# Kernel tuning notes

Measured on AMD Instinct MI355X. Metric: run time of the kernel, lower is better.

## Reference

```python
import jax, jax.numpy as jnp
import numpy as np

H = 8                 # num_heads
SCALE = 25.0          # self.scale
SIM_THRESH = 0.75
CONF_SIM_THRESH = 0.99


def _l2n(x):
    return x / jnp.linalg.norm(x, axis=-1, keepdims=True)


def setup_inputs() -> dict:
    key = jax.random.key(0)
    ks = jax.random.split(key, 10)
    B, N1, N2, C = 1, 512, 2048, 1024
    s = 0.02
    return {
        'x_cls': jax.random.normal(ks[0], (B, N2, C), jnp.float32),
        'x_reg': jax.random.normal(ks[1], (B, N2, C), jnp.float32),
        'cls_score': jax.random.uniform(ks[2], (N2,), dtype=jnp.float32),
        'fg_score': jax.random.uniform(ks[3], (N2,), dtype=jnp.float32),
        'W_q_cls': jax.random.normal(ks[4], (C, C), jnp.float32) * s,
        'W_kv_cls': jax.random.normal(ks[5], (C, 2 * C), jnp.float32) * s,
        'W_q_reg': jax.random.normal(ks[6], (C, C), jnp.float32) * s,
        'W_kv_reg': jax.random.normal(ks[7], (C, 2 * C), jnp.float32) * s,
        'W_lin': jax.random.normal(ks[8], (2 * C, 2 * C), jnp.float32) * s,
        'b_lin': jnp.zeros((2 * C,), jnp.float32),
        'W_lin_reg': jax.random.normal(ks[9], (2 * C, 2 * C), jnp.float32) * s,
        'b_lin_reg': jnp.zeros((2 * C,), jnp.float32),
        'local_preds_num': 512,
    }


def _forward(x_cls, x_reg, cls_score, fg_score, W_q_cls, W_kv_cls, W_q_reg, W_kv_reg,
             W_lin, b_lin, W_lin_reg, b_lin_reg, N1):
    B, N2, C = x_cls.shape
    hd = C // H
    # QKV projections (torch Linear with bias=False; weights stored [in,out])
    q_cls = (x_cls[:, :N1] @ W_q_cls).reshape(B, N1, H, hd).transpose(0, 2, 1, 3)   # [B,H,N1,hd]
    kv = (x_cls @ W_kv_cls).reshape(B, N2, 2, H, hd).transpose(2, 0, 3, 1, 4)
    k_cls, v_cls = kv[0], kv[1]                                                      # [B,H,N2,hd]
    q_reg = (x_reg[:, :N1] @ W_q_reg).reshape(B, N1, H, hd).transpose(0, 2, 1, 3)
    kv = (x_reg @ W_kv_reg).reshape(B, N2, 2, H, hd).transpose(2, 0, 3, 1, 4)
    k_reg, v_reg = kv[0], kv[1]
    # L2 normalization of q, k and of v for raw similarity
    q_cls, k_cls = _l2n(q_cls), _l2n(k_cls)
    q_reg, k_reg = _l2n(q_reg), _l2n(k_reg)
    v_cls_n, v_reg_n = _l2n(v_cls), _l2n(v_reg)
    # per-key score broadcast over [1,H,N1,N2] (use_mask=False path)
    cs = cls_score.reshape(1, 1, 1, N2)
    # raw value-value similarity
    attn_cls_raw = jnp.einsum('bhqd,bhkd->bhqk', v_cls_n[:, :, :N1], v_cls_n)        # [B,H,N1,N2]
    attn_reg_raw = jnp.einsum('bhqd,bhkd->bhqk', v_reg_n[:, :, :N1], v_reg_n)
    # blended softmax attention (attn_drop=0 -> identity)
    attn_cls = jax.nn.softmax(jnp.einsum('bhqd,bhkd->bhqk', q_cls, k_cls) * SCALE * cs, axis=-1)
    attn_reg = jax.nn.softmax(jnp.einsum('bhqd,bhkd->bhqk', q_reg, k_reg) * SCALE, axis=-1)
    attn = (attn_cls + attn_reg) * 0.5
    # attended features + original local values, then output linears
    x = jnp.einsum('bhqk,bhkd->bhqd', attn, v_cls).transpose(0, 2, 1, 3).reshape(B, N1, C)
    x_ori = v_cls[:, :, :N1].transpose(0, 2, 1, 3).reshape(B, N1, C)
    out_cls = jnp.concatenate([x, x_ori], axis=-1) @ W_lin + b_lin                   # [B,N1,2C]
    xr = jnp.einsum('bhqk,bhkd->bhqd', attn, v_reg).transpose(0, 2, 1, 3).reshape(B, N1, C)
    xr_ori = v_reg[:, :, :N1].transpose(0, 2, 1, 3).reshape(B, N1, C)
    out_reg = jnp.concatenate([xr, xr_ori], axis=-1) @ W_lin_reg + b_lin_reg         # reconf=True
    # ave branch: similarity-masked renormalized second-round averaging (batch 0)
    sim_mask = (attn_cls_raw.sum(axis=1)[0] / H > SIM_THRESH).astype(x_cls.dtype)    # [N1,N2]
    obj_mask = (attn_reg_raw.sum(axis=1)[0] / H > CONF_SIM_THRESH).astype(x_cls.dtype)
    sim_round2 = jax.nn.softmax(attn.sum(axis=1)[0] / H, axis=-1)
    sim_round2 = sim_mask * sim_round2
    sim_round2 = sim_round2 / sim_round2.sum(axis=-1, keepdims=True)
    obj_w = obj_mask * sim_round2
    obj_w = obj_w / obj_w.sum(axis=-1, keepdims=True)
    support_cls = v_cls.transpose(0, 2, 1, 3).reshape(B, N2, C)[0]                   # [N2,C]
    support_reg = v_reg.transpose(0, 2, 1, 3).reshape(B, N2, C)[0]
    cls_feature = jnp.concatenate([sim_round2 @ support_cls, out_cls[0]], axis=-1)   # [N1,3C]
    reg_feature = jnp.concatenate([obj_w @ support_reg, out_reg[0]], axis=-1)        # [N1,3C]
    return cls_feature, reg_feature


def reference(x_cls, x_reg, cls_score, fg_score, W_q_cls, W_kv_cls, W_q_reg, W_kv_reg,
              W_lin, b_lin, W_lin_reg, b_lin_reg, local_preds_num):
    return _forward(x_cls, x_reg, cls_score, fg_score, W_q_cls, W_kv_cls, W_q_reg,
                    W_kv_reg, W_lin, b_lin, W_lin_reg, b_lin_reg, local_preds_num)
```

## Files before the change

### kernel.cpp

```cpp
#include <hip/hip_runtime.h>

typedef _Float16 half8 __attribute__((ext_vector_type(8)));
typedef _Float16 half4v __attribute__((ext_vector_type(4)));
typedef float f32x4 __attribute__((ext_vector_type(4)));

#define GLD16(gptr, lptr) \
    __builtin_amdgcn_global_load_lds((const __attribute__((address_space(1))) void*)(gptr), \
                                     (__attribute__((address_space(3))) void*)(lptr), 16, 0, 0)

#define WAIT_VM3   0x0F73
#define WAIT_VM0   0x0F70
#define WAIT_LGKM0 0xC07F

struct GD {
    const _Float16* A; const _Float16* B; void* C;
    const float* colScale;
    _Float16 *vnp, *vtp, *xop;
    long sAh, sAg, sBh, sBg, sSplit, sCh, sCg;
    int lda, ldb, ldc, K, SK, hmask, hshift;
    int ahx, outHalf, csMode, nx, ny, normMode;
    float alpha;
};

__global__ __launch_bounds__(512, 4)
void hgemm3(GD d0, GD d1, int zSplit)
{
    const bool second = (int)blockIdx.z >= zSplit;
    const GD& d = second ? d1 : d0;
    const int bz = second ? (int)blockIdx.z - zSplit : (int)blockIdx.z;
    const int bx = (int)blockIdx.x, by = (int)blockIdx.y;
    if (bx >= d.nx || by >= d.ny) return;

    __shared__ uint4 smem[4608];
    char* sb = (char*)smem;
    const int tid = threadIdx.x;
    const int w = tid >> 6, l = tid & 63;
    const int m0 = by << 8, n0 = bx << 7;
    const int wm = (w >> 1) << 6, wn = (w & 1) << 6;
    const int kq = l >> 4, lm = l & 15;

    const int zz = bz / d.SK, s = bz - zz * d.SK;
    const int h = d.ahx ? bx : (zz & d.hmask);
    const int g = d.ahx ? zz : (zz >> d.hshift);
    const _Float16* A = d.A + (long)h * d.sAh + (long)g * d.sAg;
    const _Float16* B = d.B + (long)h * d.sBh + (long)g * d.sBg;
    const long Coff = (long)s * d.sSplit + (long)h * d.sCh + (long)g * d.sCg;
    const int kper = d.K / d.SK, kbeg = s * kper;
    const int NT = kper >> 5;

    const int rS = (w << 4) + (l >> 2);
    const int cS = (l & 3) ^ ((l >> 3) & 3);
    const _Float16* gA0 = A + (long)(m0 + rS) * d.lda + kbeg + cS * 8;
    const _Float16* gB0 = B + (long)(n0 + rS) * d.ldb + kbeg + cS * 8;
    const int lo = w * 1024 + l * 16;

    auto stage = [&](int t) {
        char* dst = sb + (t % 3) * 24576;
        GLD16(gA0 + t * 32,                     dst + lo);
        GLD16(gA0 + (long)128 * d.lda + t * 32, dst + 8192 + lo);
        GLD16(gB0 + t * 32,                     dst + 16384 + lo);
    };

    f32x4 acc[4][4] = {};
    stage(0);
    if (NT > 1) stage(1);
    if (NT > 1) __builtin_amdgcn_s_waitcnt(WAIT_VM3);
    else        __builtin_amdgcn_s_waitcnt(WAIT_VM0);
    __builtin_amdgcn_s_barrier();

    const int sw16 = ((kq ^ ((lm >> 1) & 3)) << 4);
    for (int t = 0; t < NT; ++t) {
        const char* cb = sb + (t % 3) * 24576;
        const char* pa = cb + (wm + lm) * 64 + sw16;
        const char* pb = cb + 16384 + (wn + lm) * 64 + sw16;
        half8 af[4], bfr[4];
        bfr[0] = *(const half8*)(pb + 0 * 1024);
        bfr[1] = *(const half8*)(pb + 1 * 1024);
        #pragma unroll
        for (int i = 0; i < 4; ++i) af[i] = *(const half8*)(pa + i * 1024);
        if (t + 2 < NT) stage(t + 2);
        __builtin_amdgcn_s_waitcnt(WAIT_LGKM0);
        __builtin_amdgcn_sched_barrier(0);
        __builtin_amdgcn_s_setprio(1);
        #pragma unroll
        for (int mi = 0; mi < 4; ++mi) {
            acc[mi][0] = __builtin_amdgcn_mfma_f32_16x16x32_f16(af[mi], bfr[0], acc[mi][0], 0, 0, 0);
            acc[mi][1] = __builtin_amdgcn_mfma_f32_16x16x32_f16(af[mi], bfr[1], acc[mi][1], 0, 0, 0);
        }
        __builtin_amdgcn_s_setprio(0);
        bfr[2] = *(const half8*)(pb + 2 * 1024);
        bfr[3] = *(const half8*)(pb + 3 * 1024);
        if (t + 2 < NT)      __builtin_amdgcn_s_waitcnt(WAIT_VM3);
        else if (t + 1 < NT) __builtin_amdgcn_s_waitcnt(WAIT_VM0);
        __builtin_amdgcn_s_waitcnt(WAIT_LGKM0);
        __builtin_amdgcn_sched_barrier(0);
        __builtin_amdgcn_s_setprio(1);
        #pragma unroll
        for (int mi = 0; mi < 4; ++mi) {
            acc[mi][2] = __builtin_amdgcn_mfma_f32_16x16x32_f16(af[mi], bfr[2], acc[mi][2], 0, 0, 0);
            acc[mi][3] = __builtin_amdgcn_mfma_f32_16x16x32_f16(af[mi], bfr[3], acc[mi][3], 0, 0, 0);
        }
        __builtin_amdgcn_s_setprio(0);
        __builtin_amdgcn_s_barrier();
    }

    if (d.normMode == 0) {
        const int rbase = m0 + wm + kq * 4;
        #pragma unroll
        for (int mi = 0; mi < 4; ++mi) {
            #pragma unroll
            for (int ni = 0; ni < 4; ++ni) {
                const int col = n0 + wn + ni * 16 + lm;
                float cs = d.alpha;
                if (d.csMode == 1 || (d.csMode == 2 && g == 0)) cs *= d.colScale[col];
                #pragma unroll
                for (int r = 0; r < 4; ++r) {
                    const long row = rbase + mi * 16 + r;
                    const float v = acc[mi][ni][r] * cs;
                    const long off = Coff + row * d.ldc + col;
                    if (d.outHalf) ((_Float16*)d.C)[off] = (_Float16)v;
                    else           ((float*)d.C)[off] = v;
                }
            }
        }
        return;
    }

    float* part = (float*)sb;
    float ssq[4][4];
    #pragma unroll
    for (int mi = 0; mi < 4; ++mi)
        #pragma unroll
        for (int r = 0; r < 4; ++r) {
            float sq = 0.f;
            #pragma unroll
            for (int ni = 0; ni < 4; ++ni) { const float v = acc[mi][ni][r]; sq += v * v; }
            sq += __shfl_xor(sq, 1, 64);
            sq += __shfl_xor(sq, 2, 64);
            sq += __shfl_xor(sq, 4, 64);
            sq += __shfl_xor(sq, 8, 64);
            ssq[mi][r] = sq;
        }
    if (lm == 0) {
        #pragma unroll
        for (int mi = 0; mi < 4; ++mi)
            #pragma unroll
            for (int r = 0; r < 4; ++r)
                part[(w & 1) * 256 + wm + kq * 4 + mi * 16 + r] = ssq[mi][r];
    }
    __syncthreads();

    #pragma unroll
    for (int mi = 0; mi < 4; ++mi) {
        #pragma unroll
        for (int r = 0; r < 4; ++r) {
            const int rl = wm + kq * 4 + mi * 16 + r;
            const float inv = rsqrtf(part[rl] + part[256 + rl]);
            const long rg = m0 + rl;
            if (d.normMode == 1) {
                #pragma unroll
                for (int ni = 0; ni < 4; ++ni) {
                    const int col = n0 + wn + ni * 16 + lm;
                    ((_Float16*)d.C)[(long)g * 524288 + rg * 1024 + col] =
                        (_Float16)(acc[mi][ni][r] * inv);
                }
            } else if (n0 < 1024) {
                #pragma unroll
                for (int ni = 0; ni < 4; ++ni) {
                    const int col = n0 + wn + ni * 16 + lm;
                    ((_Float16*)d.C)[(long)g * 2097152 + rg * 1024 + col] =
                        (_Float16)(acc[mi][ni][r] * inv);
                }
            } else {
                #pragma unroll
                for (int ni = 0; ni < 4; ++ni) {
                    const int nL = n0 - 1024 + wn + ni * 16 + lm;
                    d.vnp[(long)g * 2097152 + rg * 1024 + nL] =
                        (_Float16)(acc[mi][ni][r] * inv);
                    if (rg < 512)
                        d.xop[(long)g * 524288 + rg * 1024 + nL] = (_Float16)acc[mi][ni][r];
                }
            }
        }
    }
    if (d.normMode == 2 && n0 >= 1024) {
        #pragma unroll
        for (int mi = 0; mi < 4; ++mi)
            #pragma unroll
            for (int ni = 0; ni < 4; ++ni) {
                const int nL = n0 - 1024 + wn + ni * 16 + lm;
                half4v t;
                t.x = (_Float16)acc[mi][ni][0]; t.y = (_Float16)acc[mi][ni][1];
                t.z = (_Float16)acc[mi][ni][2]; t.w = (_Float16)acc[mi][ni][3];
                *(half4v*)(d.vtp + (long)g * 2097152 + (long)nL * 2048
                           + m0 + wm + kq * 4 + mi * 16) = t;
            }
    }
}

static GD mkgd(const _Float16* A, const _Float16* B, void* C, const float* cscale,
               long sAh, long sAg, long sBh, long sBg, long sSplit, long sCh, long sCg,
               int lda, int ldb, int ldc, int K, int SK, int hmask, int hshift,
               int ahx, int outHalf, int csMode, int nx, int ny, float alpha)
{
    GD d; d.A=A; d.B=B; d.C=C; d.colScale=cscale;
    d.vnp=nullptr; d.vtp=nullptr; d.xop=nullptr;
    d.sAh=sAh; d.sAg=sAg; d.sBh=sBh; d.sBg=sBg; d.sSplit=sSplit; d.sCh=sCh; d.sCg=sCg;
    d.lda=lda; d.ldb=ldb; d.ldc=ldc; d.K=K; d.SK=SK; d.hmask=hmask; d.hshift=hshift;
    d.ahx=ahx; d.outHalf=outHalf; d.csMode=csMode; d.nx=nx; d.ny=ny; d.normMode=0;
    d.alpha=alpha;
    return d;
}

__global__ __launch_bounds__(256)
void prep_all(const float* __restrict__ x_cls, const float* __restrict__ x_reg,
              const float* __restrict__ Wq_c, const float* __restrict__ Wq_r,
              const float* __restrict__ Wkv_c, const float* __restrict__ Wkv_r,
              const float* __restrict__ Wl_c, const float* __restrict__ Wl_r,
              _Float16* __restrict__ xbf,
              _Float16* __restrict__ WqT, _Float16* __restrict__ WkvT,
              _Float16* __restrict__ WlinT)
{
    const int z = blockIdx.z;
    if (z == 6) {
        const int lin = blockIdx.y * 64 + blockIdx.x;
        const int which = lin >> 11;
        const int i = (lin & 2047) * 256 + threadIdx.x;
        const float* s = which ? x_reg : x_cls;
        const float4 v = ((const float4*)s)[i];
        half4v o;
        o.x = (_Float16)v.x; o.y = (_Float16)v.y; o.z = (_Float16)v.z; o.w = (_Float16)v.w;
        ((half4v*)(xbf + (size_t)which * 2097152))[i] = o;
        return;
    }
    __shared__ float t[32][33];
    const float* src; _Float16* dst; int ldsrc, lddst, nx, ky;
    switch (z) {
        case 0: src=Wq_c;  dst=WqT;            ldsrc=1024; lddst=1024; nx=32; ky=32; break;
        case 1: src=Wq_r;  dst=WqT+1048576;    ldsrc=1024; lddst=1024; nx=32; ky=32; break;
        case 2: src=Wkv_c; dst=WkvT;           ldsrc=2048; lddst=1024; nx=64; ky=32; break;
        case 3: src=Wkv_r; dst=WkvT+2097152;   ldsrc=2048; lddst=1024; nx=64; ky=32; break;
        case 4: src=Wl_c;  dst=WlinT;          ldsrc=2048; lddst=2048; nx=64; ky=64; break;
        default:src=Wl_r;  dst=WlinT+4194304;  ldsrc=2048; lddst=2048; nx=64; ky=64; break;
    }
    if ((int)blockIdx.x >= nx || (int)blockIdx.y >= ky) return;
    const int n0 = blockIdx.x << 5, k0 = blockIdx.y << 5;
    const int tx = threadIdx.x & 31, ty = threadIdx.x >> 5;
    #pragma unroll
    for (int j = ty; j < 32; j += 8)
        t[j][tx] = src[(size_t)(k0 + j) * ldsrc + n0 + tx];
    __syncthreads();
    #pragma unroll
    for (int j = ty; j < 32; j += 8)
        dst[(size_t)(n0 + j) * lddst + k0 + tx] = (_Float16)t[tx][j];
}

template<int OP>
__device__ __forceinline__ float bred(float v, float* lds)
{
    #pragma unroll
    for (int o = 32; o > 0; o >>= 1) {
        const float u = __shfl_xor(v, o, 64);
        v = OP ? fmaxf(v, u) : v + u;
    }
    __syncthreads();
    if ((threadIdx.x & 63) == 0) lds[threadIdx.x >> 6] = v;
    __syncthreads();
    return OP ? fmaxf(fmaxf(lds[0], lds[1]), fmaxf(lds[2], lds[3]))
              : lds[0] + lds[1] + lds[2] + lds[3];
}

template<int OP>
__device__ __forceinline__ void bred2(float& a, float& b, float* lds)
{
    #pragma unroll
    for (int o = 32; o > 0; o >>= 1) {
        const float ua = __shfl_xor(a, o, 64);
        const float ub = __shfl_xor(b, o, 64);
        a = OP ? fmaxf(a, ua) : a + ua;
        b = OP ? fmaxf(b, ub) : b + ub;
    }
    __syncthreads();
    if ((threadIdx.x & 63) == 0) {
        const int wi = threadIdx.x >> 6;
        lds[wi] = a; lds[4 + wi] = b;
    }
    __syncthreads();
    a = OP ? fmaxf(fmaxf(lds[0], lds[1]), fmaxf(lds[2], lds[3]))
           : lds[0] + lds[1] + lds[2] + lds[3];
    b = OP ? fmaxf(fmaxf(lds[4], lds[5]), fmaxf(lds[6], lds[7]))
           : lds[4] + lds[5] + lds[6] + lds[7];
}

__global__ __launch_bounds__(256)
void sb2_kernel(const _Float16* __restrict__ S16, const float* __restrict__ simPart,
                _Float16* __restrict__ attn,
                _Float16* __restrict__ wc, _Float16* __restrict__ wr)
{
    __shared__ float lds[8];
    const int q = blockIdx.x, t = threadIdx.x;
    const int c0 = t * 8;
    float asum[8] = {};
    for (int hh = 0; hh < 8; ++hh) {
        const size_t rb = (size_t)(hh * 512 + q) * 2048 + c0;
        const half8 hc = *(const half8*)(S16 + rb);
        const half8 hr = *(const half8*)(S16 + 8388608 + rb);
        float vc[8], vr[8];
        float mc = -1e30f, mr = -1e30f;
        #pragma unroll
        for (int j = 0; j < 8; ++j) {
            vc[j] = (float)hc[j]; vr[j] = (float)hr[j];
            mc = fmaxf(mc, vc[j]); mr = fmaxf(mr, vr[j]);
        }
        bred2<1>(mc, mr, lds);
        float sc = 0.f, sr = 0.f;
        #pragma unroll
        for (int j = 0; j < 8; ++j) {
            vc[j] = expf(vc[j] - mc); sc += vc[j];
            vr[j] = expf(vr[j] - mr); sr += vr[j];
        }
        bred2<0>(sc, sr, lds);
        const float ic = 0.5f / sc, ir = 0.5f / sr;
        half8 oa;
        #pragma unroll
        for (int j = 0; j < 8; ++j) {
            const float a = vc[j] * ic + vr[j] * ir;
            oa[j] = (_Float16)a;
            asum[j] += a;
        }
        *(half8*)(attn + rb) = oa;
    }
    float mx = -1e30f;
    #pragma unroll
    for (int j = 0; j < 8; ++j) { asum[j] *= 0.125f; mx = fmaxf(mx, asum[j]); }
    mx = bred<1>(mx, lds);
    const size_t qb = (size_t)q * 2048 + c0;
    const float4 sa = *(const float4*)(simPart + qb);
    const float4 sb_ = *(const float4*)(simPart + qb + 4);
    const float4 ra = *(const float4*)(simPart + 1048576 + qb);
    const float4 rb_ = *(const float4*)(simPart + 1048576 + qb + 4);
    const float sim[8] = {sa.x, sa.y, sa.z, sa.w, sb_.x, sb_.y, sb_.z, sb_.w};
    const float reg[8] = {ra.x, ra.y, ra.z, ra.w, rb_.x, rb_.y, rb_.z, rb_.w};
    float em[8], emo[8];
    float s1 = 0.f, s2 = 0.f;
    #pragma unroll
    for (int j = 0; j < 8; ++j) {
        const float e = expf(asum[j] - mx);
        const float m  = sim[j] > 0.75f ? 1.f : 0.f;
        const float mo = reg[j] > 0.99f ? 1.f : 0.f;
        em[j] = e * m; emo[j] = e * m * mo;
        s1 += em[j]; s2 += emo[j];
    }
    bred2<0>(s1, s2, lds);
    const float i1 = 1.f / s1, i2 = 1.f / s2;
    half8 o1, o2;
    #pragma unroll
    for (int j = 0; j < 8; ++j) {
        o1[j] = (_Float16)(em[j] * i1);
        o2[j] = (_Float16)(emo[j] * i2);
    }
    *(half8*)(wc + qb) = o1;
    *(half8*)(wr + qb) = o2;
}

__global__ __launch_bounds__(256)
void build_xcat(const _Float16* __restrict__ xcatPart, const _Float16* __restrict__ x_ori,
                _Float16* __restrict__ xcat)
{
    const int v8 = blockIdx.x * 256 + threadIdx.x;
    const size_t base = (size_t)v8 * 8;
    const int j = (int)(base & 2047);
    const int n = (int)((base >> 11) & 511);
    const int g = (int)(base >> 20);
    half8 o;
    if (j < 1024) {
        const size_t p = (size_t)g * 524288 + (size_t)n * 1024 + j;
        float a[8] = {};
        #pragma unroll
        for (int s = 0; s < 4; ++s) {
            const half8 v = *(const half8*)(xcatPart + (size_t)s * 1048576 + p);
            #pragma unroll
            for (int k = 0; k < 8; ++k) a[k] += (float)v[k];
        }
        #pragma unroll
        for (int k = 0; k < 8; ++k) o[k] = (_Float16)a[k];
    } else {
        o = *(const half8*)(x_ori + (size_t)g * 524288 + (size_t)n * 1024 + (j - 1024));
    }
    *(half8*)(xcat + base) = o;
}

__global__ __launch_bounds__(256)
void finalize(const float* __restrict__ avePart, const float* __restrict__ outPart,
              const float* __restrict__ b_lin, const float* __restrict__ b_lin_reg,
              float* __restrict__ out)
{
    const int v4 = blockIdx.x * 256 + threadIdx.x;
    const size_t base = (size_t)v4 * 4;
    const int c = (int)(base % 3072);
    const int r = (int)((base / 3072) & 511);
    const int g = (int)(base / (3072 * 512));
    float4 v;
    if (c < 1024) {
        const size_t p = (size_t)g * 524288 + (size_t)r * 1024 + c;
        v = make_float4(0.f, 0.f, 0.f, 0.f);
        #pragma unroll
        for (int s = 0; s < 4; ++s) {
            const float4 u = *(const float4*)(avePart + (size_t)s * 1048576 + p);
            v.x += u.x; v.y += u.y; v.z += u.z; v.w += u.w;
        }
    } else {
        const int cc = c - 1024;
        v = *(const float4*)((g ? b_lin_reg : b_lin) + cc);
        const size_t p = (size_t)g * 1048576 + (size_t)r * 2048 + cc;
        #pragma unroll
        for (int s = 0; s < 4; ++s) {
            const float4 u = *(const float4*)(outPart + (size_t)s * 2097152 + p);
            v.x += u.x; v.y += u.y; v.z += u.z; v.w += u.w;
        }
    }
    *(float4*)(out + base) = v;
}

extern "C" void kernel_launch(void* const* d_in, const int* in_sizes, int n_in,
                              void* d_out, int out_size, void* d_ws, size_t ws_size,
                              hipStream_t stream)
{
    const float* x_cls     = (const float*)d_in[0];
    const float* x_reg     = (const float*)d_in[1];
    const float* cls_score = (const float*)d_in[2];
    const float* W_q_cls   = (const float*)d_in[4];
    const float* W_kv_cls  = (const float*)d_in[5];
    const float* W_q_reg   = (const float*)d_in[6];
    const float* W_kv_reg  = (const float*)d_in[7];
    const float* W_lin     = (const float*)d_in[8];
    const float* b_lin     = (const float*)d_in[9];
    const float* W_lin_reg = (const float*)d_in[10];
    const float* b_lin_reg = (const float*)d_in[11];
    float* out = (float*)d_out;

    if (ws_size < (size_t)124 * 1048576) return;

    char* W = (char*)d_ws;
    auto at = [&](size_t mb) { return (void*)(W + mb * 1048576); };
    _Float16* WlinT   = (_Float16*)at(0);
    _Float16* vT      = (_Float16*)at(16);
    _Float16* x_ori   = (_Float16*)at(24);
    _Float16* w_c     = (_Float16*)at(26);
    _Float16* w_r     = (_Float16*)at(28);
    _Float16* qn      = (_Float16*)at(30);
    float*    simPart = (float*)at(32);
    float*    outPart = (float*)at(32);
    _Float16* kn      = (_Float16*)at(40);
    _Float16* vn      = (_Float16*)at(48);
    _Float16* attn_h  = (_Float16*)at(40);
    _Float16* xbf     = (_Float16*)at(56);
    _Float16* WqT     = (_Float16*)at(64);
    _Float16* xcat16  = (_Float16*)at(64);
    _Float16* WkvT    = (_Float16*)at(68);
    _Float16* S16     = (_Float16*)at(76);
    _Float16* xcatPart= (_Float16*)at(76);
    float*    avePart = (float*)at(84);

    prep_all<<<dim3(64, 64, 7), 256, 0, stream>>>(
        x_cls, x_reg, W_q_cls, W_q_reg, W_kv_cls, W_kv_reg, W_lin, W_lin_reg,
        xbf, WqT, WkvT, WlinT);

    {
        GD q  = mkgd(xbf, WqT, qn, nullptr,
                     0, 2097152, 0, 1048576, 0, 0, 0,
                     1024, 1024, 1024, 1024, 1, 0, 0, 1, 0, 0, 8, 2, 1.f);
        q.normMode = 1;
        GD kv = mkgd(xbf, WkvT, kn, nullptr,
                     0, 2097152, 0, 2097152, 0, 0, 0,
                     1024, 1024, 1024, 1024, 1, 0, 0, 1, 0, 0, 16, 8, 1.f);
        kv.normMode = 2; kv.vnp = vn; kv.vtp = vT; kv.xop = x_ori;
        hgemm3<<<dim3(16, 8, 4), 512, 0, stream>>>(q, kv, 2);
    }

    {
        GD vs = mkgd(vn, vn, simPart, nullptr,
                     0, 2097152, 0, 2097152, 0, 0, 1048576,
                     1024, 1024, 2048, 1024, 1, 0, 0, 0, 0, 0, 16, 2, 0.125f);
        GD sc = mkgd(qn, kn, S16, cls_score,
                     128, 524288, 128, 2097152, 0, 1048576, 8388608,
                     1024, 1024, 2048, 128, 1, 7, 3, 0, 1, 2, 16, 2, 25.f);
        hgemm3<<<dim3(16, 2, 18), 512, 0, stream>>>(vs, sc, 2);
    }

    sb2_kernel<<<512, 256, 0, stream>>>(S16, simPart, attn_h, w_c, w_r);

    {
        GD av = mkgd(attn_h, vT, xcatPart, nullptr,
                     1048576, 0, 0, 2097152, 1048576, 0, 524288,
                     2048, 2048, 1024, 2048, 4, 0, 0, 1, 1, 0, 8, 2, 1.f);
        GD ae = mkgd(w_c, vT, avePart, nullptr,
                     0, 1048576, 0, 2097152, 1048576, 0, 524288,
                     2048, 2048, 1024, 2048, 4, 0, 0, 0, 0, 0, 8, 2, 1.f);
        hgemm3<<<dim3(8, 2, 16), 512, 0, stream>>>(av, ae, 8);
    }

    build_xcat<<<1024, 256, 0, stream>>>(xcatPart, x_ori, xcat16);

    {
        GD ol = mkgd(xcat16, WlinT, outPart, nullptr,
                     0, 1048576, 0, 4194304, 2097152, 0, 1048576,
                     2048, 2048, 2048, 2048, 4, 0, 0, 0, 0, 0, 16, 2, 1.f);
        hgemm3<<<dim3(16, 2, 8), 512, 0, stream>>>(ol, ol, 8);
    }

    finalize<<<3072, 256, 0, stream>>>(avePart, outPart, b_lin, b_lin_reg, out);
}
```

Baseline: 270.1 us.

## Write x_ori directly into xcat buffer and simplify GEMM main loop schedule

The KV projection epilogue now writes the unnormalized V rows straight into the right half of the concatenated xcat buffer, so build_xcat only reduces the split-K partials into the left half. This drops the separate x_ori buffer and halves build_xcat's grid and traffic. The GEMM inner loop is also rewritten to load all A/B fragments at once and issue all 16 MFMAs together. It drops the split half-step schedule, sched_barriers and setprio, and issues the next stage's global loads after the MFMAs instead of before them. That may reduce overlap between LDS reads, global prefetch and MFMA work.

```diff
diff --git a/kernel.cpp b/kernel.cpp
--- a/kernel.cpp
+++ b/kernel.cpp
@@ -71,36 +71,22 @@
     const int sw16 = ((kq ^ ((lm >> 1) & 3)) << 4);
     for (int t = 0; t < NT; ++t) {
         const char* cb = sb + (t % 3) * 24576;
+        half8 af[4], bfr[4];
         const char* pa = cb + (wm + lm) * 64 + sw16;
         const char* pb = cb + 16384 + (wn + lm) * 64 + sw16;
-        half8 af[4], bfr[4];
-        bfr[0] = *(const half8*)(pb + 0 * 1024);
-        bfr[1] = *(const half8*)(pb + 1 * 1024);
-        #pragma unroll
-        for (int i = 0; i < 4; ++i) af[i] = *(const half8*)(pa + i * 1024);
-        if (t + 2 < NT) stage(t + 2);
+        #pragma unroll
+        for (int i = 0; i < 4; ++i) {
+            af[i]  = *(const half8*)(pa + i * 1024);
+            bfr[i] = *(const half8*)(pb + i * 1024);
+        }
+        #pragma unroll
+        for (int mi = 0; mi < 4; ++mi)
+            #pragma unroll
+            for (int ni = 0; ni < 4; ++ni)
+                acc[mi][ni] = __builtin_amdgcn_mfma_f32_16x16x32_f16(af[mi], bfr[ni], acc[mi][ni], 0, 0, 0);
         __builtin_amdgcn_s_waitcnt(WAIT_LGKM0);
-        __builtin_amdgcn_sched_barrier(0);
-        __builtin_amdgcn_s_setprio(1);
-        #pragma unroll
-        for (int mi = 0; mi < 4; ++mi) {
-            acc[mi][0] = __builtin_amdgcn_mfma_f32_16x16x32_f16(af[mi], bfr[0], acc[mi][0], 0, 0, 0);
-            acc[mi][1] = __builtin_amdgcn_mfma_f32_16x16x32_f16(af[mi], bfr[1], acc[mi][1], 0, 0, 0);
-        }
-        __builtin_amdgcn_s_setprio(0);
-        bfr[2] = *(const half8*)(pb + 2 * 1024);
-        bfr[3] = *(const half8*)(pb + 3 * 1024);
-        if (t + 2 < NT)      __builtin_amdgcn_s_waitcnt(WAIT_VM3);
+        if (t + 2 < NT) { stage(t + 2); __builtin_amdgcn_s_waitcnt(WAIT_VM3); }
         else if (t + 1 < NT) __builtin_amdgcn_s_waitcnt(WAIT_VM0);
-        __builtin_amdgcn_s_waitcnt(WAIT_LGKM0);
-        __builtin_amdgcn_sched_barrier(0);
-        __builtin_amdgcn_s_setprio(1);
-        #pragma unroll
-        for (int mi = 0; mi < 4; ++mi) {
-            acc[mi][2] = __builtin_amdgcn_mfma_f32_16x16x32_f16(af[mi], bfr[2], acc[mi][2], 0, 0, 0);
-            acc[mi][3] = __builtin_amdgcn_mfma_f32_16x16x32_f16(af[mi], bfr[3], acc[mi][3], 0, 0, 0);
-        }
-        __builtin_amdgcn_s_setprio(0);
         __builtin_amdgcn_s_barrier();
     }
 
@@ -178,7 +164,8 @@
                     d.vnp[(long)g * 2097152 + rg * 1024 + nL] =
                         (_Float16)(acc[mi][ni][r] * inv);
                     if (rg < 512)
-                        d.xop[(long)g * 524288 + rg * 1024 + nL] = (_Float16)acc[mi][ni][r];
+                        d.xop[((long)g * 512 + rg) * 2048 + 1024 + nL] =
+                            (_Float16)acc[mi][ni][r];
                 }
             }
         }
@@ -364,30 +351,24 @@
 }
 
 __global__ __launch_bounds__(256)
-void build_xcat(const _Float16* __restrict__ xcatPart, const _Float16* __restrict__ x_ori,
-                _Float16* __restrict__ xcat)
+void build_xcat(const _Float16* __restrict__ xcatPart, _Float16* __restrict__ xcat)
 {
     const int v8 = blockIdx.x * 256 + threadIdx.x;
-    const size_t base = (size_t)v8 * 8;
-    const int j = (int)(base & 2047);
-    const int n = (int)((base >> 11) & 511);
-    const int g = (int)(base >> 20);
+    const int g = v8 >> 16;
+    const int n = (v8 >> 7) & 511;
+    const int j = (v8 & 127) * 8;
+    const size_t p = (size_t)g * 524288 + (size_t)n * 1024 + j;
+    float a[8] = {};
+    #pragma unroll
+    for (int s = 0; s < 4; ++s) {
+        const half8 v = *(const half8*)(xcatPart + (size_t)s * 1048576 + p);
+        #pragma unroll
+        for (int k = 0; k < 8; ++k) a[k] += (float)v[k];
+    }
     half8 o;
-    if (j < 1024) {
-        const size_t p = (size_t)g * 524288 + (size_t)n * 1024 + j;
-        float a[8] = {};
-        #pragma unroll
-        for (int s = 0; s < 4; ++s) {
-            const half8 v = *(const half8*)(xcatPart + (size_t)s * 1048576 + p);
-            #pragma unroll
-            for (int k = 0; k < 8; ++k) a[k] += (float)v[k];
-        }
-        #pragma unroll
-        for (int k = 0; k < 8; ++k) o[k] = (_Float16)a[k];
-    } else {
-        o = *(const half8*)(x_ori + (size_t)g * 524288 + (size_t)n * 1024 + (j - 1024));
-    }
-    *(half8*)(xcat + base) = o;
+    #pragma unroll
+    for (int k = 0; k < 8; ++k) o[k] = (_Float16)a[k];
+    *(half8*)(xcat + ((size_t)g * 512 + n) * 2048 + j) = o;
 }
 
 __global__ __launch_bounds__(256)
@@ -445,7 +426,6 @@
     auto at = [&](size_t mb) { return (void*)(W + mb * 1048576); };
     _Float16* WlinT   = (_Float16*)at(0);
     _Float16* vT      = (_Float16*)at(16);
-    _Float16* x_ori   = (_Float16*)at(24);
     _Float16* w_c     = (_Float16*)at(26);
     _Float16* w_r     = (_Float16*)at(28);
     _Float16* qn      = (_Float16*)at(30);
@@ -456,11 +436,11 @@
     _Float16* attn_h  = (_Float16*)at(40);
     _Float16* xbf     = (_Float16*)at(56);
     _Float16* WqT     = (_Float16*)at(64);
-    _Float16* xcat16  = (_Float16*)at(64);
     _Float16* WkvT    = (_Float16*)at(68);
     _Float16* S16     = (_Float16*)at(76);
     _Float16* xcatPart= (_Float16*)at(76);
     float*    avePart = (float*)at(84);
+    _Float16* xcat16  = (_Float16*)at(108);
 
     prep_all<<<dim3(64, 64, 7), 256, 0, stream>>>(
         x_cls, x_reg, W_q_cls, W_q_reg, W_kv_cls, W_kv_reg, W_lin, W_lin_reg,
@@ -474,7 +454,7 @@
         GD kv = mkgd(xbf, WkvT, kn, nullptr,
                      0, 2097152, 0, 2097152, 0, 0, 0,
                      1024, 1024, 1024, 1024, 1, 0, 0, 1, 0, 0, 16, 8, 1.f);
-        kv.normMode = 2; kv.vnp = vn; kv.vtp = vT; kv.xop = x_ori;
+        kv.normMode = 2; kv.vnp = vn; kv.vtp = vT; kv.xop = xcat16;
         hgemm3<<<dim3(16, 8, 4), 512, 0, stream>>>(q, kv, 2);
     }
 
@@ -500,7 +480,7 @@
         hgemm3<<<dim3(8, 2, 16), 512, 0, stream>>>(av, ae, 8);
     }
 
-    build_xcat<<<1024, 256, 0, stream>>>(xcatPart, x_ori, xcat16);
+    build_xcat<<<512, 256, 0, stream>>>(xcatPart, xcat16);
 
     {
         GD ol = mkgd(xcat16, WlinT, outPart, nullptr,
```

New measurement: 275.8 us. 1.02x slower.
